# Kernel tuning notes

Measured on AMD Instinct MI355X. Metric: run time of the kernel, lower is better.

## Reference

```python
import jax, jax.numpy as jnp
import numpy as np

B = 16384
S0, S1 = 7, 7
NB, NC = 2, 20
WC, WN = 5.0, 0.5  # weight_coord, weight_noobject
D = NB * 5 + NC  # 30


def setup_inputs() -> dict:
    key = jax.random.key(0)
    k1, k2, k3, k4 = jax.random.split(key, 4)
    predication = jax.random.normal(k1, (B, S0 * S1 * D), dtype=jnp.float32)
    grid = jax.random.randint(k2, (B, S0, S1), 0, 2, dtype=jnp.int32)
    tbox = jax.random.uniform(k3, (B, S0, S1, 4), dtype=jnp.float32)
    # keep target w,h strictly positive (real boxes), offsets in [0,1)
    tbox = tbox.at[..., 2:].set(0.05 + 0.9 * tbox[..., 2:])
    tcls = jax.random.randint(k4, (B, S0, S1), 0, NC, dtype=jnp.int32)
    return {"predication": predication, "grid": grid, "tbox": tbox, "tcls": tcls}


def _yolo_loss(predication, grid, tbox, tcls):
    pred = predication.reshape(B, S0, S1, D)
    conf = jax.nn.sigmoid(pred[..., :NB])                                  # (B,S0,S1,NB)
    pb = jax.nn.sigmoid(pred[..., NB:5 * NB]).reshape(B, S0, S1, NB, 4)    # (B,S0,S1,NB,4)
    cls = jax.nn.softmax(pred[..., 5 * NB:], axis=-1)                      # (B,S0,S1,NC)

    # cell coordinates: x = column index, y = row index (matches the [1,0] swap in torch code)
    xg = jnp.arange(S1, dtype=pred.dtype)[None, None, :]   # (1,1,S1)
    yg = jnp.arange(S0, dtype=pred.dtype)[None, :, None]   # (1,S0,1)

    tox, toy, tw, th = tbox[..., 0], tbox[..., 1], tbox[..., 2], tbox[..., 3]
    tcx = (xg + tox) / S0
    tcy = (yg + toy) / S1

    pcx = (xg[..., None] + pb[..., 0]) / S0   # (B,S0,S1,NB)
    pcy = (yg[..., None] + pb[..., 1]) / S1
    pw, ph = pb[..., 2], pb[..., 3]

    # IOU of each predicted box vs the cell's target box (same formula as _calc_iou)
    tb_ = jnp.minimum(tcx[..., None] + tw[..., None] / 2, pcx + pw / 2) - \
          jnp.maximum(tcx[..., None] - tw[..., None] / 2, pcx - pw / 2)
    lr_ = jnp.minimum(tcy[..., None] + th[..., None] / 2, pcy + ph / 2) - \
          jnp.maximum(tcy[..., None] - th[..., None] / 2, pcy - ph / 2)
    inter = jnp.where((tb_ < 0) | (lr_ < 0), 0.0, tb_ * lr_)
    iou = inter / ((tw * th)[..., None] + pw * ph - inter)                 # (B,S0,S1,NB)

    # best predictor chosen on detached IOUs (original uses pred_boxes.detach())
    best = jnp.argmax(jax.lax.stop_gradient(iou), axis=-1)                 # (B,S0,S1)

    take = lambda a: jnp.take_along_axis(a, best[..., None], axis=-1)[..., 0]
    iou_b = take(iou)          # attached IOU re-used in confidence loss
    conf_b = take(conf)
    pbb = jnp.take_along_axis(pb, best[..., None, None], axis=3)[..., 0, :]  # (B,S0,S1,4)

    cls_t = jnp.take_along_axis(cls, tcls[..., None], axis=-1)[..., 0]

    coord = (pbb[..., 0] - tox) ** 2 + (pbb[..., 1] - toy) ** 2 \
          + (jnp.sqrt(pbb[..., 2]) - jnp.sqrt(tw)) ** 2 \
          + (jnp.sqrt(pbb[..., 3]) - jnp.sqrt(th)) ** 2

    obj_loss = WC * coord + (conf_b - iou_b) ** 2 + (1.0 - cls_t) ** 2     # (B,S0,S1)
    noobj_loss = WN * jnp.sum(conf ** 2, axis=-1)                          # (B,S0,S1)

    objm = (grid == 1).astype(pred.dtype)
    total = jnp.sum(objm * obj_loss + (1.0 - objm) * noobj_loss)
    return total / B


def reference(predication, grid, tbox, tcls):
    return _yolo_loss(predication, grid, tbox, tcls)
```

## Files before the change

kernel.cpp:

```cpp
#include <hip/hip_runtime.h>
#include <math.h>

namespace {

constexpr int kB    = 16384;
constexpr int kS0   = 7;
constexpr int kS1   = 7;
constexpr int kD    = 30;
constexpr int kCells = kB * kS0 * kS1;
constexpr int TPB   = 256;
constexpr int CPB   = 256;
constexpr int NBLK  = kCells / CPB;
constexpr int TILE_F  = CPB * kD;
constexpr int TILE_V4 = TILE_F / 4;
constexpr int LSTRIDE = kD + 1;
constexpr float kInv7 = 1.0f / 7.0f;
constexpr float kWC = 5.0f;
constexpr float kWN = 0.5f;

__device__ __forceinline__ float frcp(float x) {
    return __builtin_amdgcn_rcpf(x);
}

__device__ __forceinline__ float sigm(float x) {
    return frcp(1.0f + __expf(-x));
}

__global__ void __launch_bounds__(TPB, 4) yolo_loss_kernel(
    const float* __restrict__ pred,
    const int*   __restrict__ grid,
    const float* __restrict__ tbox,
    const int*   __restrict__ tcls,
    float* __restrict__ partials)
{
    __shared__ float sp[CPB * LSTRIDE];
    __shared__ float wsum[TPB / 64];

    const int tid  = threadIdx.x;
    const int cell = blockIdx.x * CPB + tid;
    const int wave = tid >> 6;
    const int lane = tid & 63;

    const float4 tb4 = reinterpret_cast<const float4*>(tbox)[cell];
    const int g  = grid[cell];
    const int tc = tcls[cell];

    const float4* __restrict__ gp4 =
        reinterpret_cast<const float4*>(pred + (size_t)blockIdx.x * TILE_F);
    #pragma unroll
    for (int k = 0; k < 8; ++k) {
        const int i = tid + k * TPB;
        if (k < 7 || i < TILE_V4) {
            const float4 v = gp4[i];
            const int L0 = 4 * i;
            const int c0 = L0 / 30;
            const int j0 = L0 - 30 * c0;
            sp[L0 + 0 + c0]                      = v.x;
            sp[L0 + 1 + c0 + ((j0 + 1) >= 30)]  = v.y;
            sp[L0 + 2 + c0 + ((j0 + 2) >= 30)]  = v.z;
            sp[L0 + 3 + c0 + ((j0 + 3) >= 30)]  = v.w;
        }
    }
    __syncthreads();

    const float* __restrict__ fb = &sp[tid * LSTRIDE];

    const int cj = cell % kS1;
    const int ci = (cell / kS1) % kS0;
    const float tox = tb4.x, toy = tb4.y, tw = tb4.z, th = tb4.w;

    const float conf0 = sigm(fb[0]);
    const float conf1 = sigm(fb[1]);
    float pbx[2], pby[2], pbw[2], pbh[2];
    #pragma unroll
    for (int k = 0; k < 2; ++k) {
        pbx[k] = sigm(fb[2 + 4 * k + 0]);
        pby[k] = sigm(fb[2 + 4 * k + 1]);
        pbw[k] = sigm(fb[2 + 4 * k + 2]);
        pbh[k] = sigm(fb[2 + 4 * k + 3]);
    }

    float csum = 0.0f, et = 0.0f;
    #pragma unroll
    for (int q = 0; q < 20; ++q) {
        const float e = __expf(fb[10 + q]);
        csum += e;
        et = (q == tc) ? e : et;
    }
    const float cls_t = et * frcp(csum);

    const float x = (float)cj, y = (float)ci;
    const float tcx = (x + tox) * kInv7;
    const float tcy = (y + toy) * kInv7;
    const float thw = tw * 0.5f, thh = th * 0.5f;
    const float tarea = tw * th;

    float iou[2];
    #pragma unroll
    for (int k = 0; k < 2; ++k) {
        const float pcx = (x + pbx[k]) * kInv7;
        const float pcy = (y + pby[k]) * kInv7;
        const float pw = pbw[k], ph = pbh[k];
        const float tb_ = fminf(tcx + thw, pcx + pw * 0.5f) - fmaxf(tcx - thw, pcx - pw * 0.5f);
        const float lr_ = fminf(tcy + thh, pcy + ph * 0.5f) - fmaxf(tcy - thh, pcy - ph * 0.5f);
        float inter = tb_ * lr_;
        inter = (tb_ < 0.0f || lr_ < 0.0f) ? 0.0f : inter;
        iou[k] = inter * frcp(tarea + pw * ph - inter);
    }

    const bool b1 = (iou[1] > iou[0]);
    const float bx = b1 ? pbx[1] : pbx[0];
    const float by = b1 ? pby[1] : pby[0];
    const float bw = b1 ? pbw[1] : pbw[0];
    const float bh = b1 ? pbh[1] : pbh[0];
    const float conf_b = b1 ? conf1 : conf0;
    const float iou_b  = b1 ? iou[1] : iou[0];

    const float dx = bx - tox;
    const float dy = by - toy;
    const float dw = sqrtf(bw) - sqrtf(tw);
    const float dh = sqrtf(bh) - sqrtf(th);
    const float coord = dx * dx + dy * dy + dw * dw + dh * dh;
    const float d1 = conf_b - iou_b;
    const float d2 = 1.0f - cls_t;
    const float obj   = kWC * coord + d1 * d1 + d2 * d2;
    const float noobj = kWN * (conf0 * conf0 + conf1 * conf1);

    float v = (g == 1) ? obj : noobj;

    #pragma unroll
    for (int off = 32; off > 0; off >>= 1) v += __shfl_down(v, off, 64);
    if (lane == 0) wsum[wave] = v;
    __syncthreads();
    if (tid == 0) {
        partials[blockIdx.x] = wsum[0] + wsum[1] + wsum[2] + wsum[3];
    }
}

__global__ void __launch_bounds__(256) finish_kernel(
    const float* __restrict__ partials, float* __restrict__ out)
{
    __shared__ float wsum[4];
    const int tid = threadIdx.x;
    float v = 0.0f;
    for (int i = tid; i < NBLK; i += 256) v += partials[i];
    #pragma unroll
    for (int off = 32; off > 0; off >>= 1) v += __shfl_down(v, off, 64);
    if ((tid & 63) == 0) wsum[tid >> 6] = v;
    __syncthreads();
    if (tid == 0) out[0] = (wsum[0] + wsum[1] + wsum[2] + wsum[3]) * (1.0f / kB);
}

}

extern "C" void kernel_launch(void* const* d_in, const int* in_sizes, int n_in,
                              void* d_out, int out_size, void* d_ws, size_t ws_size,
                              hipStream_t stream) {
    const float* pred = (const float*)d_in[0];
    const int*   grid = (const int*)d_in[1];
    const float* tbox = (const float*)d_in[2];
    const int*   tcls = (const int*)d_in[3];
    float* out      = (float*)d_out;
    float* partials = (float*)d_ws;

    yolo_loss_kernel<<<NBLK, TPB, 0, stream>>>(pred, grid, tbox, tcls, partials);
    finish_kernel<<<1, 256, 0, stream>>>(partials, out);
}
```

Baseline: 163.6 us.

## Stage prediction tile via direct global-to-LDS loads and reduce with atomics

```diff
diff --git a/kernel.cpp b/kernel.cpp
--- a/kernel.cpp
+++ b/kernel.cpp
@@ -13,7 +13,6 @@
 constexpr int NBLK  = kCells / CPB;
 constexpr int TILE_F  = CPB * kD;
 constexpr int TILE_V4 = TILE_F / 4;
-constexpr int LSTRIDE = kD + 1;
 constexpr float kInv7 = 1.0f / 7.0f;
 constexpr float kWC = 5.0f;
 constexpr float kWN = 0.5f;
@@ -26,14 +25,25 @@
     return frcp(1.0f + __expf(-x));
 }
 
-__global__ void __launch_bounds__(TPB, 4) yolo_loss_kernel(
+__device__ __forceinline__ void load_lds16(const float4* g, float* lds) {
+    __builtin_amdgcn_global_load_lds(
+        (const __attribute__((address_space(1))) void*)g,
+        (__attribute__((address_space(3))) void*)lds,
+        16, 0, 0);
+}
+
+__global__ void zero_kernel(float* __restrict__ out) {
+    if (threadIdx.x == 0) out[0] = 0.0f;
+}
+
+__global__ void __launch_bounds__(TPB, 5) yolo_loss_kernel(
     const float* __restrict__ pred,
     const int*   __restrict__ grid,
     const float* __restrict__ tbox,
     const int*   __restrict__ tcls,
-    float* __restrict__ partials)
+    float* __restrict__ out)
 {
-    __shared__ float sp[CPB * LSTRIDE];
+    __shared__ float sp[TILE_F];
     __shared__ float wsum[TPB / 64];
 
     const int tid  = threadIdx.x;
@@ -48,22 +58,14 @@
     const float4* __restrict__ gp4 =
         reinterpret_cast<const float4*>(pred + (size_t)blockIdx.x * TILE_F);
     #pragma unroll
-    for (int k = 0; k < 8; ++k) {
-        const int i = tid + k * TPB;
-        if (k < 7 || i < TILE_V4) {
-            const float4 v = gp4[i];
-            const int L0 = 4 * i;
-            const int c0 = L0 / 30;
-            const int j0 = L0 - 30 * c0;
-            sp[L0 + 0 + c0]                      = v.x;
-            sp[L0 + 1 + c0 + ((j0 + 1) >= 30)]  = v.y;
-            sp[L0 + 2 + c0 + ((j0 + 2) >= 30)]  = v.z;
-            sp[L0 + 3 + c0 + ((j0 + 3) >= 30)]  = v.w;
+    for (int b = 0; b < 8; ++b) {
+        if (b < 7 || wave < 2) {
+            load_lds16(gp4 + b * 256 + tid, &sp[b * 1024 + wave * 256]);
         }
     }
     __syncthreads();
 
-    const float* __restrict__ fb = &sp[tid * LSTRIDE];
+    const float* __restrict__ fb = &sp[tid * kD];
 
     const int cj = cell % kS1;
     const int ci = (cell / kS1) % kS0;
@@ -133,22 +135,8 @@
     if (lane == 0) wsum[wave] = v;
     __syncthreads();
     if (tid == 0) {
-        partials[blockIdx.x] = wsum[0] + wsum[1] + wsum[2] + wsum[3];
+        atomicAdd(out, (wsum[0] + wsum[1] + wsum[2] + wsum[3]) * (1.0f / kB));
     }
-}
-
-__global__ void __launch_bounds__(256) finish_kernel(
-    const float* __restrict__ partials, float* __restrict__ out)
-{
-    __shared__ float wsum[4];
-    const int tid = threadIdx.x;
-    float v = 0.0f;
-    for (int i = tid; i < NBLK; i += 256) v += partials[i];
-    #pragma unroll
-    for (int off = 32; off > 0; off >>= 1) v += __shfl_down(v, off, 64);
-    if ((tid & 63) == 0) wsum[tid >> 6] = v;
-    __syncthreads();
-    if (tid == 0) out[0] = (wsum[0] + wsum[1] + wsum[2] + wsum[3]) * (1.0f / kB);
 }
 
 }
@@ -160,9 +148,8 @@
     const int*   grid = (const int*)d_in[1];
     const float* tbox = (const float*)d_in[2];
     const int*   tcls = (const int*)d_in[3];
-    float* out      = (float*)d_out;
-    float* partials = (float*)d_ws;
+    float* out = (float*)d_out;
 
-    yolo_loss_kernel<<<NBLK, TPB, 0, stream>>>(pred, grid, tbox, tcls, partials);
-    finish_kernel<<<1, 256, 0, stream>>>(partials, out);
+    zero_kernel<<<1, 64, 0, stream>>>(out);
+    yolo_loss_kernel<<<NBLK, TPB, 0, stream>>>(pred, grid, tbox, tcls, out);
 }
```

New measurement: 170.4 us. 1.04x slower.
